# Optimization experiments

Measured on AMD Instinct MI355X. Metric: run time of the kernel, lower is better.

Reference implementation:

```python
import jax, jax.numpy as jnp
import numpy as np

# Graph sizes: users -> items ('ui') and users -> tags ('ut'), plus reverse etypes.
N_U, N_I, N_T, D = 100000, 50000, 20000, 128
E_UI, E_UT = 500000, 300000


def setup_inputs() -> dict:
    key = jax.random.key(0)
    k = jax.random.split(key, 7)
    return {
        "h_u": jax.random.normal(k[0], (N_U, D), jnp.float32),
        "h_i": jax.random.normal(k[1], (N_I, D), jnp.float32),
        "h_t": jax.random.normal(k[2], (N_T, D), jnp.float32),
        "ui_src": jax.random.randint(k[3], (E_UI,), 0, N_U, jnp.int32),
        "ui_dst": jax.random.randint(k[4], (E_UI,), 0, N_I, jnp.int32),
        "ut_src": jax.random.randint(k[5], (E_UT,), 0, N_U, jnp.int32),
        "ut_dst": jax.random.randint(k[6], (E_UT,), 0, N_T, jnp.int32),
    }


def _seg_sum(x, idx, n):
    return jax.ops.segment_sum(x, idx, num_segments=n)


def _deg(idx, n):
    # in-degree, clamped to min 1 (as torch .clamp(min=1))
    return jnp.clip(_seg_sum(jnp.ones(idx.shape, jnp.float32), idx, n), 1.0, None)


def reference(h_u, h_i, h_t, ui_src, ui_dst, ut_src, ut_dst):
    NORM_2 = -1.0  # default norm_2 arg
    # forward pass: copy_u('h') + sum per etype, then 1/in_degree normalization on dst
    rst_i = _seg_sum(h_u[ui_src], ui_dst, N_I) / _deg(ui_dst, N_I)[:, None]  # [N_I, D]
    rst_t = _seg_sum(h_u[ut_src], ut_dst, N_T) / _deg(ut_dst, N_T)[:, None]  # [N_T, D]
    # backward pass: multi_update_all over reverse etypes, 'sum' cross-etype reducer
    bsrc = _seg_sum(rst_i[ui_dst], ui_src, N_U) + _seg_sum(rst_t[ut_dst], ut_src, N_U)
    # in_degrees_b: per-etype clamped degrees summed across reverse etypes
    deg_b = _deg(ui_src, N_U) + _deg(ut_src, N_U)
    bsrc = bsrc * (deg_b ** NORM_2)[:, None]
    # rst is the LAST etype's normalized dst result ('ut' -> tags)
    return bsrc, rst_t
```

## Files before the change

### kernel.cpp

```cpp
#include <hip/hip_runtime.h>

#define NU 100000
#define NI 50000
#define NT 20000
#define DD 128
#define EUI 500000
#define EUT 300000

#define B_I   0
#define B_T   (NI)
#define B_UUI (NI + NT)
#define B_UUT (NI + NT + NU)
#define NSCAN (NI + NT + NU + NU)
#define TOTAL_E (2 * (EUI + EUT))

#define BPB   512
#define NB    ((NSCAN + BPB - 1) / BPB)
#define CH    8192
#define NBLK  ((TOTAL_E + CH - 1) / CH)
#define NT3   176

__device__ __forceinline__ unsigned bfpack(float a, float b) {
    unsigned ua = __float_as_uint(a), ub = __float_as_uint(b);
    ua = (ua + 0x7FFFu + ((ua >> 16) & 1u)) >> 16;
    ub = (ub + 0x7FFFu + ((ub >> 16) & 1u)) >> 16;
    return ua | (ub << 16);
}
__device__ __forceinline__ void bacc(unsigned p, float& a, float& b) {
    a += __uint_as_float(p << 16);
    b += __uint_as_float(p & 0xFFFF0000u);
}

__device__ __forceinline__ int bucket_of(int e,
        const int* __restrict__ ui_src, const int* __restrict__ ui_dst,
        const int* __restrict__ ut_src, const int* __restrict__ ut_dst) {
    if (e < EUI)               return B_I   + ui_dst[e];
    if (e < 2 * EUI)           return B_UUI + ui_src[e - EUI];
    if (e < 2 * EUI + EUT)     return B_T   + ut_dst[e - 2 * EUI];
    return B_UUT + ut_src[e - 2 * EUI - EUT];
}

__device__ __forceinline__ void entry_of(int e,
        const int* __restrict__ ui_src, const int* __restrict__ ui_dst,
        const int* __restrict__ ut_src, const int* __restrict__ ut_dst,
        int& bucket, int& val) {
    if (e < EUI)               { bucket = B_I   + ui_dst[e];               val = ui_src[e]; }
    else if (e < 2 * EUI)      { int j = e - EUI;           bucket = B_UUI + ui_src[j]; val = ui_dst[j]; }
    else if (e < 2 * EUI + EUT){ int j = e - 2 * EUI;       bucket = B_T   + ut_dst[j]; val = ut_src[j]; }
    else                       { int j = e - 2 * EUI - EUT; bucket = B_UUT + ut_src[j]; val = ut_dst[j]; }
}

__global__ void k_hist2(const int* __restrict__ ui_src, const int* __restrict__ ui_dst,
                        const int* __restrict__ ut_src, const int* __restrict__ ut_dst,
                        int* __restrict__ gbin) {
    __shared__ int h[NB];
    int b = blockIdx.x, t = threadIdx.x;
    for (int i = t; i < NB; i += 256) h[i] = 0;
    __syncthreads();
    int e0 = b * CH;
    int e1 = min(e0 + CH, TOTAL_E);
    for (int e = e0 + t; e < e1; e += 256)
        atomicAdd(&h[bucket_of(e, ui_src, ui_dst, ut_src, ut_dst) >> 9], 1);
    __syncthreads();
    for (int i = t; i < NB; i += 256)
        if (h[i]) atomicAdd(&gbin[i], h[i]);
}

__global__ void k_scan528(const int* __restrict__ gbin,
                          int* __restrict__ gstart, int* __restrict__ cursor) {
    __shared__ int tsum[256];
    int t = threadIdx.x;
    int i = t * 3;
    int v0 = 0, v1 = 0, v2 = 0;
    if (t < NT3) { v0 = gbin[i]; v1 = gbin[i + 1]; v2 = gbin[i + 2]; }
    int s = v0 + v1 + v2;
    tsum[t] = s;
    __syncthreads();
    for (int o = 1; o < 256; o <<= 1) {
        int x = (t >= o) ? tsum[t - o] : 0;
        __syncthreads();
        tsum[t] += x;
        __syncthreads();
    }
    int base = tsum[t] - s;
    if (t < NT3) {
        gstart[i] = base;                cursor[i] = base;
        gstart[i + 1] = base + v0;       cursor[i + 1] = base + v0;
        gstart[i + 2] = base + v0 + v1;  cursor[i + 2] = base + v0 + v1;
    }
    if (t == 255) gstart[NB] = tsum[255];
}

__global__ void k_scatterbin2(const int* __restrict__ ui_src, const int* __restrict__ ui_dst,
                              const int* __restrict__ ut_src, const int* __restrict__ ut_dst,
                              int* __restrict__ cursor, unsigned* __restrict__ binned) {
    __shared__ int h[NB];
    int b = blockIdx.x, t = threadIdx.x;
    for (int i = t; i < NB; i += 256) h[i] = 0;
    __syncthreads();
    int e0 = b * CH;
    int e1 = min(e0 + CH, TOTAL_E);
    for (int e = e0 + t; e < e1; e += 256)
        atomicAdd(&h[bucket_of(e, ui_src, ui_dst, ut_src, ut_dst) >> 9], 1);
    __syncthreads();
    for (int i = t; i < NB; i += 256) {
        int c = h[i];
        if (c) h[i] = atomicAdd(&cursor[i], c);
    }
    __syncthreads();
    for (int e = e0 + t; e < e1; e += 256) {
        int bucket, val;
        entry_of(e, ui_src, ui_dst, ut_src, ut_dst, bucket, val);
        int pos = atomicAdd(&h[bucket >> 9], 1);
        binned[pos] = ((unsigned)(bucket & (BPB - 1)) << 17) | (unsigned)val;
    }
}

__global__ void k_fine(const unsigned* __restrict__ binned, const int* __restrict__ gstart,
                       int* __restrict__ off, int* __restrict__ edges) {
    __shared__ int cnt[BPB];
    __shared__ int tsum[256];
    int b = blockIdx.x, t = threadIdx.x;
    cnt[t] = 0; cnt[t + 256] = 0;
    __syncthreads();
    int s = gstart[b], e = gstart[b + 1];
    for (int i = s + t; i < e; i += 256) atomicAdd(&cnt[binned[i] >> 17], 1);
    __syncthreads();
    int v0 = cnt[2 * t], v1 = cnt[2 * t + 1];
    int ps = v0 + v1;
    tsum[t] = ps;
    __syncthreads();
    for (int o = 1; o < 256; o <<= 1) {
        int x = (t >= o) ? tsum[t - o] : 0;
        __syncthreads();
        tsum[t] += x;
        __syncthreads();
    }
    int base = s + tsum[t] - ps;
    int g0 = b * BPB + 2 * t;
    if (g0 < NSCAN) off[g0] = base;
    if (g0 + 1 < NSCAN) off[g0 + 1] = base + v0;
    __syncthreads();
    cnt[2 * t] = base;
    cnt[2 * t + 1] = base + v0;
    __syncthreads();
    for (int i = s + t; i < e; i += 256) {
        unsigned v = binned[i];
        int pos = atomicAdd(&cnt[v >> 17], 1);
        edges[pos] = (int)(v & 0x1FFFFu);
    }
}

__global__ void k_cvt(const float4* __restrict__ in, uint4* __restrict__ out) {
    int t = blockIdx.x * blockDim.x + threadIdx.x;
    if (t >= NU * DD / 8) return;
    float4 a = in[t * 2 + 0];
    float4 b = in[t * 2 + 1];
    uint4 o;
    o.x = bfpack(a.x, a.y); o.y = bfpack(a.z, a.w);
    o.z = bfpack(b.x, b.y); o.w = bfpack(b.z, b.w);
    out[t] = o;
}

__device__ __forceinline__ void gacc16(const uint4* __restrict__ feat,
                                       const int* __restrict__ edges,
                                       int start, int end, int c,
                                       float& a0, float& a1, float& a2, float& a3,
                                       float& a4, float& a5, float& a6, float& a7) {
    for (int base = start; base < end; base += 16) {
        int n = end - base; if (n > 16) n = 16;
        int eidx = (c < n) ? edges[base + c] : 0;
        int k = 0;
        for (; k + 8 <= n; k += 8) {
            int s0 = __shfl(eidx, k + 0, 16), s1 = __shfl(eidx, k + 1, 16);
            int s2 = __shfl(eidx, k + 2, 16), s3 = __shfl(eidx, k + 3, 16);
            int s4 = __shfl(eidx, k + 4, 16), s5 = __shfl(eidx, k + 5, 16);
            int s6 = __shfl(eidx, k + 6, 16), s7 = __shfl(eidx, k + 7, 16);
            uint4 p0 = feat[(size_t)s0 * 16 + c], p1 = feat[(size_t)s1 * 16 + c];
            uint4 p2 = feat[(size_t)s2 * 16 + c], p3 = feat[(size_t)s3 * 16 + c];
            uint4 p4 = feat[(size_t)s4 * 16 + c], p5 = feat[(size_t)s5 * 16 + c];
            uint4 p6 = feat[(size_t)s6 * 16 + c], p7 = feat[(size_t)s7 * 16 + c];
            bacc(p0.x, a0, a1); bacc(p0.y, a2, a3); bacc(p0.z, a4, a5); bacc(p0.w, a6, a7);
            bacc(p1.x, a0, a1); bacc(p1.y, a2, a3); bacc(p1.z, a4, a5); bacc(p1.w, a6, a7);
            bacc(p2.x, a0, a1); bacc(p2.y, a2, a3); bacc(p2.z, a4, a5); bacc(p2.w, a6, a7);
            bacc(p3.x, a0, a1); bacc(p3.y, a2, a3); bacc(p3.z, a4, a5); bacc(p3.w, a6, a7);
            bacc(p4.x, a0, a1); bacc(p4.y, a2, a3); bacc(p4.z, a4, a5); bacc(p4.w, a6, a7);
            bacc(p5.x, a0, a1); bacc(p5.y, a2, a3); bacc(p5.z, a4, a5); bacc(p5.w, a6, a7);
            bacc(p6.x, a0, a1); bacc(p6.y, a2, a3); bacc(p6.z, a4, a5); bacc(p6.w, a6, a7);
            bacc(p7.x, a0, a1); bacc(p7.y, a2, a3); bacc(p7.z, a4, a5); bacc(p7.w, a6, a7);
        }
        for (; k + 2 <= n; k += 2) {
            int s0 = __shfl(eidx, k + 0, 16), s1 = __shfl(eidx, k + 1, 16);
            uint4 p0 = feat[(size_t)s0 * 16 + c], p1 = feat[(size_t)s1 * 16 + c];
            bacc(p0.x, a0, a1); bacc(p0.y, a2, a3); bacc(p0.z, a4, a5); bacc(p0.w, a6, a7);
            bacc(p1.x, a0, a1); bacc(p1.y, a2, a3); bacc(p1.z, a4, a5); bacc(p1.w, a6, a7);
        }
        if (k < n) {
            int s0 = __shfl(eidx, k, 16);
            uint4 p0 = feat[(size_t)s0 * 16 + c];
            bacc(p0.x, a0, a1); bacc(p0.y, a2, a3); bacc(p0.z, a4, a5); bacc(p0.w, a6, a7);
        }
    }
}

__global__ void g_fwd(const uint4* __restrict__ feat,
                      const int* __restrict__ off, const int* __restrict__ edges,
                      uint4* __restrict__ rsti_b, uint4* __restrict__ rstt_b,
                      float4* __restrict__ outf) {
    int tid = blockIdx.x * blockDim.x + threadIdx.x;
    int r = tid >> 4;
    int c = tid & 15;
    if (r >= NI + NT) return;
    int start = off[r];
    int end = off[r + 1];
    float a0=0.f,a1=0.f,a2=0.f,a3=0.f,a4=0.f,a5=0.f,a6=0.f,a7=0.f;
    gacc16(feat, edges, start, end, c, a0, a1, a2, a3, a4, a5, a6, a7);
    float inv = 1.0f / fmaxf((float)(end - start), 1.0f);
    a0*=inv; a1*=inv; a2*=inv; a3*=inv; a4*=inv; a5*=inv; a6*=inv; a7*=inv;
    uint4 ob;
    ob.x = bfpack(a0,a1); ob.y = bfpack(a2,a3);
    ob.z = bfpack(a4,a5); ob.w = bfpack(a6,a7);
    if (r < NI) {
        rsti_b[(size_t)r * 16 + c] = ob;
    } else {
        int rt = r - NI;
        rstt_b[(size_t)rt * 16 + c] = ob;
        float4 f0; f0.x=a0; f0.y=a1; f0.z=a2; f0.w=a3;
        float4 f1; f1.x=a4; f1.y=a5; f1.z=a6; f1.w=a7;
        outf[(size_t)rt * 32 + c*2 + 0] = f0;
        outf[(size_t)rt * 32 + c*2 + 1] = f1;
    }
}

__global__ void g_bwd(const uint4* __restrict__ rst_i, const uint4* __restrict__ rst_t,
                      const int* __restrict__ off, const int* __restrict__ edges,
                      float4* __restrict__ bsrc) {
    int tid = blockIdx.x * blockDim.x + threadIdx.x;
    int r = tid >> 4;
    int c = tid & 15;
    if (r >= NU) return;
    int s1 = off[B_UUI + r], e1 = off[B_UUI + r + 1];
    int g2 = B_UUT + r;
    int s2 = off[g2], e2 = (g2 + 1 < NSCAN) ? off[g2 + 1] : TOTAL_E;
    float a0=0.f,a1=0.f,a2=0.f,a3=0.f,a4=0.f,a5=0.f,a6=0.f,a7=0.f;
    gacc16(rst_i, edges, s1, e1, c, a0, a1, a2, a3, a4, a5, a6, a7);
    gacc16(rst_t, edges, s2, e2, c, a0, a1, a2, a3, a4, a5, a6, a7);
    float inv = 1.0f / (fmaxf((float)(e1 - s1), 1.0f) + fmaxf((float)(e2 - s2), 1.0f));
    float4 f0; f0.x=a0*inv; f0.y=a1*inv; f0.z=a2*inv; f0.w=a3*inv;
    float4 f1; f1.x=a4*inv; f1.y=a5*inv; f1.z=a6*inv; f1.w=a7*inv;
    bsrc[(size_t)r * 32 + c*2 + 0] = f0;
    bsrc[(size_t)r * 32 + c*2 + 1] = f1;
}

__global__ void k_scanA(int* __restrict__ data, int* __restrict__ bsums, int n) {
    __shared__ int lds[256];
    int b = blockIdx.x, t = threadIdx.x;
    int base = b * 1024 + t * 4;
    int v0 = (base + 0 < n) ? data[base + 0] : 0;
    int v1 = (base + 1 < n) ? data[base + 1] : 0;
    int v2 = (base + 2 < n) ? data[base + 2] : 0;
    int v3 = (base + 3 < n) ? data[base + 3] : 0;
    int i0 = v0, i1 = i0 + v1, i2 = i1 + v2, i3 = i2 + v3;
    lds[t] = i3;
    __syncthreads();
    for (int o = 1; o < 256; o <<= 1) {
        int x = (t >= o) ? lds[t - o] : 0;
        __syncthreads();
        lds[t] += x;
        __syncthreads();
    }
    int ex = lds[t] - i3;
    if (base + 0 < n) data[base + 0] = ex + i0;
    if (base + 1 < n) data[base + 1] = ex + i1;
    if (base + 2 < n) data[base + 2] = ex + i2;
    if (base + 3 < n) data[base + 3] = ex + i3;
    if (t == 255) bsums[b] = lds[255];
}

__global__ void k_scanB(int* __restrict__ bsums, int nsb) {
    __shared__ int lds[512];
    int t = threadIdx.x;
    int a = (t < nsb) ? bsums[t] : 0;
    int b2 = (t + 256 < nsb) ? bsums[t + 256] : 0;
    lds[t] = a;
    lds[t + 256] = b2;
    __syncthreads();
    for (int o = 1; o < 512; o <<= 1) {
        int x0 = (t >= o) ? lds[t - o] : 0;
        int x1 = (t + 256 >= o) ? lds[t + 256 - o] : 0;
        __syncthreads();
        lds[t] += x0;
        lds[t + 256] += x1;
        __syncthreads();
    }
    if (t < nsb) bsums[t] = lds[t] - a;
    if (t + 256 < nsb) bsums[t + 256] = lds[t + 256] - b2;
}

__global__ void k_scanC(int* __restrict__ data, const int* __restrict__ bsums, int n) {
    int b = blockIdx.x;
    int add = bsums[b];
    int base = b * 1024 + threadIdx.x * 4;
    if (base + 0 < n) data[base + 0] += add;
    if (base + 1 < n) data[base + 1] += add;
    if (base + 2 < n) data[base + 2] += add;
    if (base + 3 < n) data[base + 3] += add;
}

__global__ void k_count_old(const int4* __restrict__ ui_src, const int4* __restrict__ ui_dst,
                            const int4* __restrict__ ut_src, const int4* __restrict__ ut_dst,
                            int* __restrict__ off) {
    int i = blockIdx.x * blockDim.x + threadIdx.x;
    if (i < EUI / 4) {
        int4 s = ui_src[i], d = ui_dst[i];
        atomicAdd(&off[B_I + d.x], 1); atomicAdd(&off[B_I + d.y], 1);
        atomicAdd(&off[B_I + d.z], 1); atomicAdd(&off[B_I + d.w], 1);
        atomicAdd(&off[B_UUI + s.x], 1); atomicAdd(&off[B_UUI + s.y], 1);
        atomicAdd(&off[B_UUI + s.z], 1); atomicAdd(&off[B_UUI + s.w], 1);
    } else if (i < EUI / 4 + EUT / 4) {
        int j = i - EUI / 4;
        int4 s = ut_src[j], d = ut_dst[j];
        atomicAdd(&off[B_T + d.x], 1); atomicAdd(&off[B_T + d.y], 1);
        atomicAdd(&off[B_T + d.z], 1); atomicAdd(&off[B_T + d.w], 1);
        atomicAdd(&off[B_UUT + s.x], 1); atomicAdd(&off[B_UUT + s.y], 1);
        atomicAdd(&off[B_UUT + s.z], 1); atomicAdd(&off[B_UUT + s.w], 1);
    }
}

__global__ void k_fill_old(const int2* __restrict__ ui_src, const int2* __restrict__ ui_dst,
                           const int2* __restrict__ ut_src, const int2* __restrict__ ut_dst,
                           int* __restrict__ off, int* __restrict__ edges) {
    int i = blockIdx.x * blockDim.x + threadIdx.x;
    if (i < EUI / 2) {
        int2 s = ui_src[i], d = ui_dst[i];
        edges[atomicAdd(&off[B_I + d.x], -1) - 1] = s.x;
        edges[atomicAdd(&off[B_UUI + s.x], -1) - 1] = d.x;
        edges[atomicAdd(&off[B_I + d.y], -1) - 1] = s.y;
        edges[atomicAdd(&off[B_UUI + s.y], -1) - 1] = d.y;
    } else if (i < EUI / 2 + EUT / 2) {
        int j = i - EUI / 2;
        int2 s = ut_src[j], d = ut_dst[j];
        edges[atomicAdd(&off[B_T + d.x], -1) - 1] = s.x;
        edges[atomicAdd(&off[B_UUT + s.x], -1) - 1] = d.x;
        edges[atomicAdd(&off[B_T + d.y], -1) - 1] = s.y;
        edges[atomicAdd(&off[B_UUT + s.y], -1) - 1] = d.y;
    }
}

__global__ void k_gather_fwd_f(const float4* __restrict__ feat,
                               const int* __restrict__ off, const int* __restrict__ edges,
                               uint2* __restrict__ outb, float4* __restrict__ outf,
                               int base, int nrows) {
    int tid = blockIdx.x * blockDim.x + threadIdx.x;
    int r = tid >> 5;
    int c = tid & 31;
    if (r >= nrows) return;
    int g = base + r;
    int start = off[g];
    int end = (g + 1 < NSCAN) ? off[g + 1] : TOTAL_E;
    float a0 = 0.f, a1 = 0.f, a2 = 0.f, a3 = 0.f;
    for (int e = start; e < end; ++e) {
        float4 v = feat[(size_t)edges[e] * 32 + c];
        a0 += v.x; a1 += v.y; a2 += v.z; a3 += v.w;
    }
    float inv = 1.0f / fmaxf((float)(end - start), 1.0f);
    a0 *= inv; a1 *= inv; a2 *= inv; a3 *= inv;
    uint2 ob; ob.x = bfpack(a0, a1); ob.y = bfpack(a2, a3);
    outb[(size_t)r * 32 + c] = ob;
    if (outf) {
        float4 of; of.x = a0; of.y = a1; of.z = a2; of.w = a3;
        outf[(size_t)r * 32 + c] = of;
    }
}

__global__ void k_gather_bwd_b(const uint2* __restrict__ rst_i,
                               const uint2* __restrict__ rst_t,
                               const int* __restrict__ off, const int* __restrict__ edges,
                               float4* __restrict__ bsrc) {
    int tid = blockIdx.x * blockDim.x + threadIdx.x;
    int r = tid >> 5;
    int c = tid & 31;
    if (r >= NU) return;
    int g1 = B_UUI + r;
    int s1 = off[g1], e1 = off[g1 + 1];
    int g2 = B_UUT + r;
    int s2 = off[g2], e2 = (g2 + 1 < NSCAN) ? off[g2 + 1] : TOTAL_E;
    float a0 = 0.f, a1 = 0.f, a2 = 0.f, a3 = 0.f;
    for (int e = s1; e < e1; ++e) {
        uint2 p = rst_i[(size_t)edges[e] * 32 + c];
        bacc(p.x, a0, a1); bacc(p.y, a2, a3);
    }
    for (int e = s2; e < e2; ++e) {
        uint2 p = rst_t[(size_t)edges[e] * 32 + c];
        bacc(p.x, a0, a1); bacc(p.y, a2, a3);
    }
    float inv = 1.0f / (fmaxf((float)(e1 - s1), 1.0f) + fmaxf((float)(e2 - s2), 1.0f));
    float4 o;
    o.x = a0 * inv; o.y = a1 * inv; o.z = a2 * inv; o.w = a3 * inv;
    bsrc[(size_t)r * 32 + c] = o;
}

__global__ void f_count(const int* __restrict__ ui_src, const int* __restrict__ ui_dst,
                        const int* __restrict__ ut_src, const int* __restrict__ ut_dst,
                        float* __restrict__ cnt_uui, float* __restrict__ cnt_i,
                        float* __restrict__ cnt_uut, float* __restrict__ cnt_t) {
    int i = blockIdx.x * blockDim.x + threadIdx.x;
    if (i < EUI) {
        unsafeAtomicAdd(&cnt_uui[ui_src[i]], 1.0f);
        unsafeAtomicAdd(&cnt_i[ui_dst[i]], 1.0f);
    } else if (i < EUI + EUT) {
        int j = i - EUI;
        unsafeAtomicAdd(&cnt_uut[ut_src[j]], 1.0f);
        unsafeAtomicAdd(&cnt_t[ut_dst[j]], 1.0f);
    }
}
__global__ void f_scatter_fwd(const float4* __restrict__ feat, const int* __restrict__ src,
                              const int* __restrict__ dst, float* __restrict__ out_sum, int nedge) {
    int tid = blockIdx.x * blockDim.x + threadIdx.x;
    int e = tid >> 5, c = tid & 31;
    if (e >= nedge) return;
    float4 v = feat[(size_t)src[e] * 32 + c];
    float* o = out_sum + (size_t)dst[e] * DD + c * 4;
    unsafeAtomicAdd(o + 0, v.x); unsafeAtomicAdd(o + 1, v.y);
    unsafeAtomicAdd(o + 2, v.z); unsafeAtomicAdd(o + 3, v.w);
}
__global__ void f_scatter_bwd(const float4* __restrict__ rst_sum, const float* __restrict__ cnt,
                              const int* __restrict__ src, const int* __restrict__ dst,
                              float* __restrict__ bsrc, int nedge) {
    int tid = blockIdx.x * blockDim.x + threadIdx.x;
    int e = tid >> 5, c = tid & 31;
    if (e >= nedge) return;
    float inv = 1.0f / fmaxf(cnt[dst[e]], 1.0f);
    float4 v = rst_sum[(size_t)dst[e] * 32 + c];
    float* o = bsrc + (size_t)src[e] * DD + c * 4;
    unsafeAtomicAdd(o + 0, v.x * inv); unsafeAtomicAdd(o + 1, v.y * inv);
    unsafeAtomicAdd(o + 2, v.z * inv); unsafeAtomicAdd(o + 3, v.w * inv);
}
__global__ void f_norm(float4* __restrict__ rst, const float* __restrict__ cnt, int nrows) {
    int tid = blockIdx.x * blockDim.x + threadIdx.x;
    int r = tid >> 5, c = tid & 31;
    if (r >= nrows) return;
    float inv = 1.0f / fmaxf(cnt[r], 1.0f);
    float4 v = rst[(size_t)r * 32 + c];
    v.x *= inv; v.y *= inv; v.z *= inv; v.w *= inv;
    rst[(size_t)r * 32 + c] = v;
}
__global__ void f_final(float4* __restrict__ bsrc, const float* __restrict__ cnt_a,
                        const float* __restrict__ cnt_b, int nrows) {
    int tid = blockIdx.x * blockDim.x + threadIdx.x;
    int r = tid >> 5, c = tid & 31;
    if (r >= nrows) return;
    float inv = 1.0f / (fmaxf(cnt_a[r], 1.0f) + fmaxf(cnt_b[r], 1.0f));
    float4 v = bsrc[(size_t)r * 32 + c];
    v.x *= inv; v.y *= inv; v.z *= inv; v.w *= inv;
    bsrc[(size_t)r * 32 + c] = v;
}


extern "C" void kernel_launch(void* const* d_in, const int* in_sizes, int n_in,
                              void* d_out, int out_size, void* d_ws, size_t ws_size,
                              hipStream_t stream) {
    const float* h_u  = (const float*)d_in[0];
    const int* ui_src = (const int*)d_in[3];
    const int* ui_dst = (const int*)d_in[4];
    const int* ut_src = (const int*)d_in[5];
    const int* ut_dst = (const int*)d_in[6];

    float* bsrc  = (float*)d_out;
    float* rst_t = (float*)d_out + (size_t)NU * DD;

    const int B = 256;

    const size_t INT_WORDS = (size_t)NSCAN + 512 + TOTAL_E;
    const size_t BASE_B    = INT_WORDS * 4;
    const size_t HUB_B     = (size_t)NU * DD * 2;
    const size_t RIB_B     = (size_t)NI * DD * 2;
    const size_t RTB_B     = (size_t)NT * DD * 2;
    const size_t NEED_FULL = BASE_B + HUB_B + RIB_B + RTB_B;
    const size_t NEED_HALF = BASE_B + RIB_B + RTB_B;

    if (ws_size >= NEED_FULL) {
        int* off      = (int*)d_ws;
        int* bsums    = off + NSCAN;   (void)bsums;
        int* edges    = bsums + 512;
        uint4* hu_b   = (uint4*)((char*)d_ws + BASE_B);
        uint4* rsti_b = (uint4*)((char*)d_ws + BASE_B + HUB_B);
        uint4* rstt_b = (uint4*)((char*)d_ws + BASE_B + HUB_B + RIB_B);
        unsigned* binned = (unsigned*)rsti_b;
        int* gbin   = (int*)rstt_b;
        int* gstart = gbin + NB;
        int* cursor = gstart + NB + 1;

        k_cvt<<<(NU * DD / 8 + B - 1) / B, B, 0, stream>>>((const float4*)h_u, hu_b);

        hipMemsetAsync(gbin, 0, NB * sizeof(int), stream);
        k_hist2<<<NBLK, B, 0, stream>>>(ui_src, ui_dst, ut_src, ut_dst, gbin);

        k_scan528<<<1, B, 0, stream>>>(gbin, gstart, cursor);

        k_scatterbin2<<<NBLK, B, 0, stream>>>(ui_src, ui_dst, ut_src, ut_dst, cursor, binned);

        k_fine<<<NB, B, 0, stream>>>(binned, gstart, off, edges);

        g_fwd<<<((long)(NI + NT) * 16 + B - 1) / B, B, 0, stream>>>(
            hu_b, off, edges, rsti_b, rstt_b, (float4*)rst_t);
        g_bwd<<<((long)NU * 16 + B - 1) / B, B, 0, stream>>>(
            rsti_b, rstt_b, off, edges, (float4*)bsrc);
    } else if (ws_size >= NEED_HALF) {
        int* off   = (int*)d_ws;
        int* bsums = off + NSCAN;
        int* edges = bsums + 512;
        uint2* rsti_b = (uint2*)((char*)d_ws + BASE_B);
        uint2* rstt_b = (uint2*)((char*)d_ws + BASE_B + RIB_B);

        hipMemsetAsync(off, 0, (NSCAN + 512) * sizeof(int), stream);

        int nq = EUI / 4 + EUT / 4;
        k_count_old<<<(nq + B - 1) / B, B, 0, stream>>>(
            (const int4*)ui_src, (const int4*)ui_dst,
            (const int4*)ut_src, (const int4*)ut_dst, off);
        {
            int nblk = (NSCAN + 1023) / 1024;
            k_scanA<<<nblk, B, 0, stream>>>(off, bsums, NSCAN);
            k_scanB<<<1, B, 0, stream>>>(bsums, nblk);
            k_scanC<<<nblk, B, 0, stream>>>(off, bsums, NSCAN);
        }
        int nh = EUI / 2 + EUT / 2;
        k_fill_old<<<(nh + B - 1) / B, B, 0, stream>>>(
            (const int2*)ui_src, (const int2*)ui_dst,
            (const int2*)ut_src, (const int2*)ut_dst, off, edges);

        k_gather_fwd_f<<<((long)NI * 32 + B - 1) / B, B, 0, stream>>>(
            (const float4*)h_u, off, edges, rsti_b, (float4*)nullptr, B_I, NI);
        k_gather_fwd_f<<<((long)NT * 32 + B - 1) / B, B, 0, stream>>>(
            (const float4*)h_u, off, edges, rstt_b, (float4*)rst_t, B_T, NT);
        k_gather_bwd_b<<<((long)NU * 32 + B - 1) / B, B, 0, stream>>>(
            rsti_b, rstt_b, off, edges, (float4*)bsrc);
    } else {
        float* ws        = (float*)d_ws;
        float* rst_i_sum = ws;
        float* cnt_i     = rst_i_sum + (size_t)NI * DD;
        float* cnt_t     = cnt_i + NI;
        float* cnt_uui   = cnt_t + NT;
        float* cnt_uut   = cnt_uui + NU;
        size_t ws_floats = (size_t)NI * DD + NI + NT + NU + NU;

        hipMemsetAsync(d_ws, 0, ws_floats * sizeof(float), stream);
        hipMemsetAsync(d_out, 0, (size_t)out_size * sizeof(float), stream);

        int n = EUI + EUT;
        f_count<<<(n + B - 1) / B, B, 0, stream>>>(ui_src, ui_dst, ut_src, ut_dst,
                                                   cnt_uui, cnt_i, cnt_uut, cnt_t);
        f_scatter_fwd<<<((long)EUI * 32 + B - 1) / B, B, 0, stream>>>(
            (const float4*)h_u, ui_src, ui_dst, rst_i_sum, EUI);
        f_scatter_fwd<<<((long)EUT * 32 + B - 1) / B, B, 0, stream>>>(
            (const float4*)h_u, ut_src, ut_dst, rst_t, EUT);
        f_scatter_bwd<<<((long)EUI * 32 + B - 1) / B, B, 0, stream>>>(
            (const float4*)rst_i_sum, cnt_i, ui_src, ui_dst, bsrc, EUI);
        f_scatter_bwd<<<((long)EUT * 32 + B - 1) / B, B, 0, stream>>>(
            (const float4*)rst_t, cnt_t, ut_src, ut_dst, bsrc, EUT);
        f_norm<<<((long)NT * 32 + B - 1) / B, B, 0, stream>>>((float4*)rst_t, cnt_t, NT);
        f_final<<<((long)NU * 32 + B - 1) / B, B, 0, stream>>>((float4*)bsrc, cnt_uui, cnt_uut, NU);
    }
}
```

Baseline: 170.7 us.

## Fuse CSR build stages into one persistent kernel with grid barriers

```diff
diff --git a/kernel.cpp b/kernel.cpp
--- a/kernel.cpp
+++ b/kernel.cpp
@@ -16,9 +16,8 @@
 
 #define BPB   512
 #define NB    ((NSCAN + BPB - 1) / BPB)
-#define CH    8192
-#define NBLK  ((TOTAL_E + CH - 1) / CH)
 #define NT3   176
+#define GFB   200
 
 __device__ __forceinline__ unsigned bfpack(float a, float b) {
     unsigned ua = __float_as_uint(a), ub = __float_as_uint(b);
@@ -29,6 +28,12 @@
 __device__ __forceinline__ void bacc(unsigned p, float& a, float& b) {
     a += __uint_as_float(p << 16);
     b += __uint_as_float(p & 0xFFFF0000u);
+}
+
+typedef float f4_t __attribute__((ext_vector_type(4)));
+__device__ __forceinline__ void nts4(float4* p, float x, float y, float z, float w) {
+    f4_t v; v.x = x; v.y = y; v.z = z; v.w = w;
+    __builtin_nontemporal_store(v, reinterpret_cast<f4_t*>(p));
 }
 
 __device__ __forceinline__ int bucket_of(int e,
@@ -48,107 +53,6 @@
     else if (e < 2 * EUI)      { int j = e - EUI;           bucket = B_UUI + ui_src[j]; val = ui_dst[j]; }
     else if (e < 2 * EUI + EUT){ int j = e - 2 * EUI;       bucket = B_T   + ut_dst[j]; val = ut_src[j]; }
     else                       { int j = e - 2 * EUI - EUT; bucket = B_UUT + ut_src[j]; val = ut_dst[j]; }
-}
-
-__global__ void k_hist2(const int* __restrict__ ui_src, const int* __restrict__ ui_dst,
-                        const int* __restrict__ ut_src, const int* __restrict__ ut_dst,
-                        int* __restrict__ gbin) {
-    __shared__ int h[NB];
-    int b = blockIdx.x, t = threadIdx.x;
-    for (int i = t; i < NB; i += 256) h[i] = 0;
-    __syncthreads();
-    int e0 = b * CH;
-    int e1 = min(e0 + CH, TOTAL_E);
-    for (int e = e0 + t; e < e1; e += 256)
-        atomicAdd(&h[bucket_of(e, ui_src, ui_dst, ut_src, ut_dst) >> 9], 1);
-    __syncthreads();
-    for (int i = t; i < NB; i += 256)
-        if (h[i]) atomicAdd(&gbin[i], h[i]);
-}
-
-__global__ void k_scan528(const int* __restrict__ gbin,
-                          int* __restrict__ gstart, int* __restrict__ cursor) {
-    __shared__ int tsum[256];
-    int t = threadIdx.x;
-    int i = t * 3;
-    int v0 = 0, v1 = 0, v2 = 0;
-    if (t < NT3) { v0 = gbin[i]; v1 = gbin[i + 1]; v2 = gbin[i + 2]; }
-    int s = v0 + v1 + v2;
-    tsum[t] = s;
-    __syncthreads();
-    for (int o = 1; o < 256; o <<= 1) {
-        int x = (t >= o) ? tsum[t - o] : 0;
-        __syncthreads();
-        tsum[t] += x;
-        __syncthreads();
-    }
-    int base = tsum[t] - s;
-    if (t < NT3) {
-        gstart[i] = base;                cursor[i] = base;
-        gstart[i + 1] = base + v0;       cursor[i + 1] = base + v0;
-        gstart[i + 2] = base + v0 + v1;  cursor[i + 2] = base + v0 + v1;
-    }
-    if (t == 255) gstart[NB] = tsum[255];
-}
-
-__global__ void k_scatterbin2(const int* __restrict__ ui_src, const int* __restrict__ ui_dst,
-                              const int* __restrict__ ut_src, const int* __restrict__ ut_dst,
-                              int* __restrict__ cursor, unsigned* __restrict__ binned) {
-    __shared__ int h[NB];
-    int b = blockIdx.x, t = threadIdx.x;
-    for (int i = t; i < NB; i += 256) h[i] = 0;
-    __syncthreads();
-    int e0 = b * CH;
-    int e1 = min(e0 + CH, TOTAL_E);
-    for (int e = e0 + t; e < e1; e += 256)
-        atomicAdd(&h[bucket_of(e, ui_src, ui_dst, ut_src, ut_dst) >> 9], 1);
-    __syncthreads();
-    for (int i = t; i < NB; i += 256) {
-        int c = h[i];
-        if (c) h[i] = atomicAdd(&cursor[i], c);
-    }
-    __syncthreads();
-    for (int e = e0 + t; e < e1; e += 256) {
-        int bucket, val;
-        entry_of(e, ui_src, ui_dst, ut_src, ut_dst, bucket, val);
-        int pos = atomicAdd(&h[bucket >> 9], 1);
-        binned[pos] = ((unsigned)(bucket & (BPB - 1)) << 17) | (unsigned)val;
-    }
-}
-
-__global__ void k_fine(const unsigned* __restrict__ binned, const int* __restrict__ gstart,
-                       int* __restrict__ off, int* __restrict__ edges) {
-    __shared__ int cnt[BPB];
-    __shared__ int tsum[256];
-    int b = blockIdx.x, t = threadIdx.x;
-    cnt[t] = 0; cnt[t + 256] = 0;
-    __syncthreads();
-    int s = gstart[b], e = gstart[b + 1];
-    for (int i = s + t; i < e; i += 256) atomicAdd(&cnt[binned[i] >> 17], 1);
-    __syncthreads();
-    int v0 = cnt[2 * t], v1 = cnt[2 * t + 1];
-    int ps = v0 + v1;
-    tsum[t] = ps;
-    __syncthreads();
-    for (int o = 1; o < 256; o <<= 1) {
-        int x = (t >= o) ? tsum[t - o] : 0;
-        __syncthreads();
-        tsum[t] += x;
-        __syncthreads();
-    }
-    int base = s + tsum[t] - ps;
-    int g0 = b * BPB + 2 * t;
-    if (g0 < NSCAN) off[g0] = base;
-    if (g0 + 1 < NSCAN) off[g0 + 1] = base + v0;
-    __syncthreads();
-    cnt[2 * t] = base;
-    cnt[2 * t + 1] = base + v0;
-    __syncthreads();
-    for (int i = s + t; i < e; i += 256) {
-        unsigned v = binned[i];
-        int pos = atomicAdd(&cnt[v >> 17], 1);
-        edges[pos] = (int)(v & 0x1FFFFu);
-    }
 }
 
 __global__ void k_cvt(const float4* __restrict__ in, uint4* __restrict__ out) {
@@ -160,6 +64,116 @@
     o.x = bfpack(a.x, a.y); o.y = bfpack(a.z, a.w);
     o.z = bfpack(b.x, b.y); o.w = bfpack(b.z, b.w);
     out[t] = o;
+}
+
+__device__ __forceinline__ void gbar(int* ctr, int target) {
+    __syncthreads();
+    if (threadIdx.x == 0) {
+        __threadfence();
+        atomicAdd(ctr, 1);
+        while (atomicAdd(ctr, 0) < target) __builtin_amdgcn_s_sleep(2);
+        __threadfence();
+    }
+    __syncthreads();
+}
+
+__global__ void k_build(const int* __restrict__ ui_src, const int* __restrict__ ui_dst,
+                        const int* __restrict__ ut_src, const int* __restrict__ ut_dst,
+                        int* __restrict__ gbin, int* __restrict__ gstart,
+                        int* __restrict__ cursor, int* __restrict__ barctr,
+                        unsigned* __restrict__ binned,
+                        int* __restrict__ off, int* __restrict__ edges) {
+    __shared__ int h[NB];
+    __shared__ int cnt[BPB];
+    __shared__ int tsum[256];
+    int bid = blockIdx.x, t = threadIdx.x;
+    const int gs = GFB * 256;
+    int gtid = bid * 256 + t;
+
+    for (int i = t; i < NB; i += 256) h[i] = 0;
+    __syncthreads();
+    for (int e = gtid; e < TOTAL_E; e += gs)
+        atomicAdd(&h[bucket_of(e, ui_src, ui_dst, ut_src, ut_dst) >> 9], 1);
+    __syncthreads();
+    for (int i = t; i < NB; i += 256)
+        if (h[i]) atomicAdd(&gbin[i], h[i]);
+
+    gbar(barctr, GFB);
+
+    if (bid == 0) {
+        int i3 = t * 3;
+        int v0 = 0, v1 = 0, v2 = 0;
+        if (t < NT3) { v0 = gbin[i3]; v1 = gbin[i3 + 1]; v2 = gbin[i3 + 2]; }
+        int s = v0 + v1 + v2;
+        tsum[t] = s;
+        __syncthreads();
+        for (int o = 1; o < 256; o <<= 1) {
+            int x = (t >= o) ? tsum[t - o] : 0;
+            __syncthreads();
+            tsum[t] += x;
+            __syncthreads();
+        }
+        int base = tsum[t] - s;
+        if (t < NT3) {
+            gstart[i3] = base;                cursor[i3] = base;
+            gstart[i3 + 1] = base + v0;       cursor[i3 + 1] = base + v0;
+            gstart[i3 + 2] = base + v0 + v1;  cursor[i3 + 2] = base + v0 + v1;
+        }
+        if (t == 255) gstart[NB] = tsum[255];
+    }
+
+    gbar(barctr, 2 * GFB);
+
+    for (int i = t; i < NB; i += 256) h[i] = 0;
+    __syncthreads();
+    for (int e = gtid; e < TOTAL_E; e += gs)
+        atomicAdd(&h[bucket_of(e, ui_src, ui_dst, ut_src, ut_dst) >> 9], 1);
+    __syncthreads();
+    for (int i = t; i < NB; i += 256) {
+        int c = h[i];
+        if (c) h[i] = atomicAdd(&cursor[i], c);
+    }
+    __syncthreads();
+    for (int e = gtid; e < TOTAL_E; e += gs) {
+        int bucket, val;
+        entry_of(e, ui_src, ui_dst, ut_src, ut_dst, bucket, val);
+        int pos = atomicAdd(&h[bucket >> 9], 1);
+        binned[pos] = ((unsigned)(bucket & (BPB - 1)) << 17) | (unsigned)val;
+    }
+
+    gbar(barctr, 3 * GFB);
+
+    for (int b = bid; b < NB; b += GFB) {
+        cnt[t] = 0; cnt[t + 256] = 0;
+        __syncthreads();
+        int s = gstart[b], e = gstart[b + 1];
+        for (int i = s + t; i < e; i += 256) atomicAdd(&cnt[binned[i] >> 17], 1);
+        __syncthreads();
+        int v0 = cnt[2 * t], v1 = cnt[2 * t + 1];
+        int ps = v0 + v1;
+        tsum[t] = ps;
+        __syncthreads();
+        for (int o = 1; o < 256; o <<= 1) {
+            int x = (t >= o) ? tsum[t - o] : 0;
+            __syncthreads();
+            tsum[t] += x;
+            __syncthreads();
+        }
+        int base = s + tsum[t] - ps;
+        int g0 = b * BPB + 2 * t;
+        if (g0 < NSCAN) off[g0] = base;
+        if (g0 + 1 < NSCAN) off[g0 + 1] = base + v0;
+        __syncthreads();
+        cnt[2 * t] = base;
+        cnt[2 * t + 1] = base + v0;
+        __syncthreads();
+        for (int i = s + t; i < e; i += 256) {
+            unsigned v = binned[i];
+            int pos = atomicAdd(&cnt[v >> 17], 1);
+            edges[pos] = (int)(v & 0x1FFFFu);
+        }
+        __syncthreads();
+    }
 }
 
 __device__ __forceinline__ void gacc16(const uint4* __restrict__ feat,
@@ -225,10 +239,8 @@
     } else {
         int rt = r - NI;
         rstt_b[(size_t)rt * 16 + c] = ob;
-        float4 f0; f0.x=a0; f0.y=a1; f0.z=a2; f0.w=a3;
-        float4 f1; f1.x=a4; f1.y=a5; f1.z=a6; f1.w=a7;
-        outf[(size_t)rt * 32 + c*2 + 0] = f0;
-        outf[(size_t)rt * 32 + c*2 + 1] = f1;
+        nts4(&outf[(size_t)rt * 32 + c*2 + 0], a0, a1, a2, a3);
+        nts4(&outf[(size_t)rt * 32 + c*2 + 1], a4, a5, a6, a7);
     }
 }
 
@@ -246,10 +258,8 @@
     gacc16(rst_i, edges, s1, e1, c, a0, a1, a2, a3, a4, a5, a6, a7);
     gacc16(rst_t, edges, s2, e2, c, a0, a1, a2, a3, a4, a5, a6, a7);
     float inv = 1.0f / (fmaxf((float)(e1 - s1), 1.0f) + fmaxf((float)(e2 - s2), 1.0f));
-    float4 f0; f0.x=a0*inv; f0.y=a1*inv; f0.z=a2*inv; f0.w=a3*inv;
-    float4 f1; f1.x=a4*inv; f1.y=a5*inv; f1.z=a6*inv; f1.w=a7*inv;
-    bsrc[(size_t)r * 32 + c*2 + 0] = f0;
-    bsrc[(size_t)r * 32 + c*2 + 1] = f1;
+    nts4(&bsrc[(size_t)r * 32 + c*2 + 0], a0*inv, a1*inv, a2*inv, a3*inv);
+    nts4(&bsrc[(size_t)r * 32 + c*2 + 1], a4*inv, a5*inv, a6*inv, a7*inv);
 }
 
 __global__ void k_scanA(int* __restrict__ data, int* __restrict__ bsums, int n) {
@@ -490,17 +500,15 @@
         int* gbin   = (int*)rstt_b;
         int* gstart = gbin + NB;
         int* cursor = gstart + NB + 1;
+        int* barctr = cursor + NB;
+
+        hipMemsetAsync(gbin, 0, (NB + (NB + 1) + NB + 1) * sizeof(int), stream);
 
         k_cvt<<<(NU * DD / 8 + B - 1) / B, B, 0, stream>>>((const float4*)h_u, hu_b);
 
-        hipMemsetAsync(gbin, 0, NB * sizeof(int), stream);
-        k_hist2<<<NBLK, B, 0, stream>>>(ui_src, ui_dst, ut_src, ut_dst, gbin);
-
-        k_scan528<<<1, B, 0, stream>>>(gbin, gstart, cursor);
-
-        k_scatterbin2<<<NBLK, B, 0, stream>>>(ui_src, ui_dst, ut_src, ut_dst, cursor, binned);
-
-        k_fine<<<NB, B, 0, stream>>>(binned, gstart, off, edges);
+        k_build<<<GFB, B, 0, stream>>>(ui_src, ui_dst, ut_src, ut_dst,
+                                       gbin, gstart, cursor, barctr,
+                                       binned, off, edges);
 
         g_fwd<<<((long)(NI + NT) * 16 + B - 1) / B, B, 0, stream>>>(
             hu_b, off, edges, rsti_b, rstt_b, (float4*)rst_t);
```

Result: slower. 225.0 us (+31.8%).

## Fuse bf16 conversion into histogram kernel, shrink edge chunks, use nontemporal output stores

Applied to the files above, without the earlier changes.

```diff
diff --git a/kernel.cpp b/kernel.cpp
--- a/kernel.cpp
+++ b/kernel.cpp
@@ -16,9 +16,10 @@
 
 #define BPB   512
 #define NB    ((NSCAN + BPB - 1) / BPB)
-#define CH    8192
+#define CH    2048
 #define NBLK  ((TOTAL_E + CH - 1) / CH)
 #define NT3   176
+#define NCVT  ((NU * DD / 8 + 255) / 256)
 
 __device__ __forceinline__ unsigned bfpack(float a, float b) {
     unsigned ua = __float_as_uint(a), ub = __float_as_uint(b);
@@ -29,6 +30,12 @@
 __device__ __forceinline__ void bacc(unsigned p, float& a, float& b) {
     a += __uint_as_float(p << 16);
     b += __uint_as_float(p & 0xFFFF0000u);
+}
+
+typedef float f4_t __attribute__((ext_vector_type(4)));
+__device__ __forceinline__ void nts4(float4* p, float x, float y, float z, float w) {
+    f4_t v; v.x = x; v.y = y; v.z = z; v.w = w;
+    __builtin_nontemporal_store(v, reinterpret_cast<f4_t*>(p));
 }
 
 __device__ __forceinline__ int bucket_of(int e,
@@ -50,11 +57,24 @@
     else                       { int j = e - 2 * EUI - EUT; bucket = B_UUT + ut_src[j]; val = ut_dst[j]; }
 }
 
-__global__ void k_hist2(const int* __restrict__ ui_src, const int* __restrict__ ui_dst,
-                        const int* __restrict__ ut_src, const int* __restrict__ ut_dst,
-                        int* __restrict__ gbin) {
+__global__ void k_cvthist(const float4* __restrict__ in, uint4* __restrict__ out,
+                          const int* __restrict__ ui_src, const int* __restrict__ ui_dst,
+                          const int* __restrict__ ut_src, const int* __restrict__ ut_dst,
+                          int* __restrict__ gbin) {
     __shared__ int h[NB];
-    int b = blockIdx.x, t = threadIdx.x;
+    if (blockIdx.x < NCVT) {
+        int t = blockIdx.x * 256 + threadIdx.x;
+        if (t < NU * DD / 8) {
+            float4 a = in[t * 2 + 0];
+            float4 b = in[t * 2 + 1];
+            uint4 o;
+            o.x = bfpack(a.x, a.y); o.y = bfpack(a.z, a.w);
+            o.z = bfpack(b.x, b.y); o.w = bfpack(b.z, b.w);
+            out[t] = o;
+        }
+        return;
+    }
+    int b = blockIdx.x - NCVT, t = threadIdx.x;
     for (int i = t; i < NB; i += 256) h[i] = 0;
     __syncthreads();
     int e0 = b * CH;
@@ -149,17 +169,6 @@
         int pos = atomicAdd(&cnt[v >> 17], 1);
         edges[pos] = (int)(v & 0x1FFFFu);
     }
-}
-
-__global__ void k_cvt(const float4* __restrict__ in, uint4* __restrict__ out) {
-    int t = blockIdx.x * blockDim.x + threadIdx.x;
-    if (t >= NU * DD / 8) return;
-    float4 a = in[t * 2 + 0];
-    float4 b = in[t * 2 + 1];
-    uint4 o;
-    o.x = bfpack(a.x, a.y); o.y = bfpack(a.z, a.w);
-    o.z = bfpack(b.x, b.y); o.w = bfpack(b.z, b.w);
-    out[t] = o;
 }
 
 __device__ __forceinline__ void gacc16(const uint4* __restrict__ feat,
@@ -225,10 +234,8 @@
     } else {
         int rt = r - NI;
         rstt_b[(size_t)rt * 16 + c] = ob;
-        float4 f0; f0.x=a0; f0.y=a1; f0.z=a2; f0.w=a3;
-        float4 f1; f1.x=a4; f1.y=a5; f1.z=a6; f1.w=a7;
-        outf[(size_t)rt * 32 + c*2 + 0] = f0;
-        outf[(size_t)rt * 32 + c*2 + 1] = f1;
+        nts4(&outf[(size_t)rt * 32 + c*2 + 0], a0, a1, a2, a3);
+        nts4(&outf[(size_t)rt * 32 + c*2 + 1], a4, a5, a6, a7);
     }
 }
 
@@ -246,10 +253,8 @@
     gacc16(rst_i, edges, s1, e1, c, a0, a1, a2, a3, a4, a5, a6, a7);
     gacc16(rst_t, edges, s2, e2, c, a0, a1, a2, a3, a4, a5, a6, a7);
     float inv = 1.0f / (fmaxf((float)(e1 - s1), 1.0f) + fmaxf((float)(e2 - s2), 1.0f));
-    float4 f0; f0.x=a0*inv; f0.y=a1*inv; f0.z=a2*inv; f0.w=a3*inv;
-    float4 f1; f1.x=a4*inv; f1.y=a5*inv; f1.z=a6*inv; f1.w=a7*inv;
-    bsrc[(size_t)r * 32 + c*2 + 0] = f0;
-    bsrc[(size_t)r * 32 + c*2 + 1] = f1;
+    nts4(&bsrc[(size_t)r * 32 + c*2 + 0], a0*inv, a1*inv, a2*inv, a3*inv);
+    nts4(&bsrc[(size_t)r * 32 + c*2 + 1], a4*inv, a5*inv, a6*inv, a7*inv);
 }
 
 __global__ void k_scanA(int* __restrict__ data, int* __restrict__ bsums, int n) {
@@ -491,10 +496,10 @@
         int* gstart = gbin + NB;
         int* cursor = gstart + NB + 1;
 
-        k_cvt<<<(NU * DD / 8 + B - 1) / B, B, 0, stream>>>((const float4*)h_u, hu_b);
-
         hipMemsetAsync(gbin, 0, NB * sizeof(int), stream);
-        k_hist2<<<NBLK, B, 0, stream>>>(ui_src, ui_dst, ut_src, ut_dst, gbin);
+
+        k_cvthist<<<NCVT + NBLK, B, 0, stream>>>(
+            (const float4*)h_u, hu_b, ui_src, ui_dst, ut_src, ut_dst, gbin);
 
         k_scan528<<<1, B, 0, stream>>>(gbin, gstart, cursor);
 
```

Result: faster. 159.6 us (median of 2 runs) (-6.5%).
